# Kernel tuning notes

Measured on AMD Instinct MI355X. Metric: run time of the kernel, lower is better.

Reference implementation:

```python
import jax, jax.numpy as jnp
import numpy as np

B, N, H, W = 128, 8192, 7, 7


def setup_inputs() -> dict:
    key = jax.random.key(0)
    ks = jax.random.split(key, 10)
    inp = {
        'x': jax.random.normal(ks[0], (B, N, H, W), dtype=jnp.float32),
        'y': jax.random.normal(ks[1], (B, N), dtype=jnp.float32),
        # nn.MultiheadAttention(embed_dim=1, num_heads=1) params (all scalar)
        'wq': jax.random.normal(ks[2], (), dtype=jnp.float32),
        'wk': jax.random.normal(ks[3], (), dtype=jnp.float32),
        'wv': jax.random.normal(ks[4], (), dtype=jnp.float32),
        'bq': jax.random.normal(ks[5], (), dtype=jnp.float32) * 0.1,
        'bk': jax.random.normal(ks[6], (), dtype=jnp.float32) * 0.1,
        'bv': jax.random.normal(ks[7], (), dtype=jnp.float32) * 0.1,
        'wo': jax.random.normal(ks[8], (), dtype=jnp.float32),
        'bo': jax.random.normal(ks[9], (), dtype=jnp.float32) * 0.1,
    }
    return inp


def _mha1(q_src, kv_src, wq, bq, wk, bk, wv, bv, wo, bo):
    # embed_dim=1, num_heads=1, scale = 1/sqrt(1) = 1.
    # torch sees (seq=B, batch=N, embed=1): attention mixes the B axis per n.
    q = q_src * wq + bq            # [B, N]
    k = kv_src * wk + bk           # [B, N]
    v = kv_src * wv + bv           # [B, N]
    scores = jnp.einsum('in,jn->ijn', q, k)      # [B, B, N]
    a = jax.nn.softmax(scores, axis=1)           # softmax over keys j
    out = jnp.einsum('ijn,jn->in', a, v)         # [B, N]
    return out * wo + bo


def reference(x, y, wq, bq, wk, bk, wv, bv, wo, bo):
    xp = jnp.mean(x, axis=(2, 3))                # AdaptiveAvgPool2d((1,1)) -> [B, N]
    self_x = _mha1(xp, xp, wq, bq, wk, bk, wv, bv, wo, bo)
    self_y = _mha1(y, y, wq, bq, wk, bk, wv, bv, wo, bo)
    cross_x = _mha1(xp, y, wq, bq, wk, bk, wv, bv, wo, bo)
    cross_y = _mha1(y, xp, wq, bq, wk, bk, wv, bv, wo, bo)
    f_x = xp + self_x
    f_y = y + self_y
    c_f_x = cross_x + f_x
    c_f_y = cross_y + f_y
    return jnp.concatenate((c_f_x, c_f_y), axis=1)   # [B, 2N]
```

## Files before the change

kernel.cpp:

```cpp
#include <hip/hip_runtime.h>


constexpr int B_SEQ = 128;
constexpr int N_COL = 8192;
constexpr int HWP   = 49;
constexpr int NT    = 256;
constexpr int TC    = 4;
constexpr int PC    = 128;

__global__ __launch_bounds__(NT) void rsca_pool(
    const float* __restrict__ x, float* __restrict__ xp)
{
    __shared__ float st[PC * HWP];
    const int t = threadIdx.x;
    const int ntiles = (B_SEQ * N_COL) / PC;
    for (int tile = blockIdx.x; tile < ntiles; tile += gridDim.x) {
        const size_t cell0 = (size_t)tile * PC;
        const float4* src = (const float4*)(x + cell0 * HWP);
        __syncthreads();
        for (int k = t; k < PC * HWP / 4; k += NT)
            ((float4*)st)[k] = src[k];
        __syncthreads();
        const int cell = t >> 1, half = t & 1;
        const float* p = st + cell * HWP + half * 25;
        float s = 0.0f;
        #pragma unroll
        for (int k = 0; k < 24; ++k) s += p[k];
        if (half == 0) s += p[24];
        s += __shfl_xor(s, 1);
        if (half == 0) xp[cell0 + cell] = s * (1.0f / HWP);
    }
}

__global__ __launch_bounds__(NT, 6) void rsca_attn(
    const float* __restrict__ xp, const float* __restrict__ y,
    const float* __restrict__ pwq, const float* __restrict__ pwk,
    const float* __restrict__ pwv, const float* __restrict__ pbq,
    const float* __restrict__ pbk, const float* __restrict__ pbv,
    const float* __restrict__ pwo, const float* __restrict__ pbo,
    float* __restrict__ out)
{
    __shared__ float2 kvxT[TC][B_SEQ];
    __shared__ float2 kvyT[TC][B_SEQ];
    __shared__ float  pmn[2][TC][8], pmx[2][TC][8];
    __shared__ float  klmn[2][TC], klmx[2][TC];

    const int t  = threadIdx.x;
    const int n0 = blockIdx.x * TC;

    const float wq = pwq[0], wk = pwk[0], wv = pwv[0];
    const float bq = pbq[0], bk = pbk[0], bv = pbv[0];
    const float wo = pwo[0], bo = pbo[0];
    const float L2E = 1.4426950408889634f;
    const float wkL = wk * L2E, bkL = bk * L2E;
    const float alpha = wo * wv;
    const float beta2 = 2.0f * (wo * bv + bo);

    for (int cell = t; cell < B_SEQ * TC; cell += NT) {
        const int j = cell >> 2, c = cell & 3;
        const float fx = xp[(size_t)j * N_COL + n0 + c];
        const float fy = y [(size_t)j * N_COL + n0 + c];
        kvxT[c][j] = make_float2(fmaf(fx, wkL, bkL), fx);
        kvyT[c][j] = make_float2(fmaf(fy, wkL, bkL), fy);
    }
    __syncthreads();

    if (t < 64) {
        const int set = t >> 5, c = (t >> 3) & 3, part = t & 7;
        float mn = 3.4e38f, mx = -3.4e38f;
        #pragma unroll
        for (int k = 0; k < 16; ++k) {
            const int j = part * 16 + k;
            const float v = set ? kvyT[c][j].x : kvxT[c][j].x;
            mn = fminf(mn, v);
            mx = fmaxf(mx, v);
        }
        pmn[set][c][part] = mn;
        pmx[set][c][part] = mx;
    }
    __syncthreads();
    if (t < 8) {
        const int set = t >> 2, c = t & 3;
        float mn = 3.4e38f, mx = -3.4e38f;
        #pragma unroll
        for (int k = 0; k < 8; ++k) {
            mn = fminf(mn, pmn[set][c][k]);
            mx = fmaxf(mx, pmx[set][c][k]);
        }
        klmn[set][c] = mn;
        klmx[set][c] = mx;
    }
    __syncthreads();

    const int i  = t & (B_SEQ - 1);
    const int ch = t >> 7;
    #pragma unroll
    for (int cc = 0; cc < 2; ++cc) {
        const int c = ch * 2 + cc;
        const float2* __restrict__ px = kvxT[c];
        const float2* __restrict__ py = kvyT[c];
        const float xi = px[i].y;
        const float yi = py[i].y;
        const float qx = fmaf(xi, wq, bq);
        const float qy = fmaf(yi, wq, bq);
        const float nmsx = -(qx >= 0.0f ? qx * klmx[0][c] : qx * klmn[0][c]);
        const float nmcy = -(qy >= 0.0f ? qy * klmx[0][c] : qy * klmn[0][c]);
        const float nmsy = -(qy >= 0.0f ? qy * klmx[1][c] : qy * klmn[1][c]);
        const float nmcx = -(qx >= 0.0f ? qx * klmx[1][c] : qx * klmn[1][c]);

        float s0sx = 0.f, s1sx = 0.f, s0cy = 0.f, s1cy = 0.f;
        float s0sy = 0.f, s1sy = 0.f, s0cx = 0.f, s1cx = 0.f;
        for (int j0 = 0; j0 < B_SEQ; j0 += 8) {
            float2 kx[8], ky[8];
            #pragma unroll
            for (int jj = 0; jj < 8; ++jj) kx[jj] = px[j0 + jj];
            #pragma unroll
            for (int jj = 0; jj < 8; ++jj) ky[jj] = py[j0 + jj];
            #pragma unroll
            for (int jj = 0; jj < 8; ++jj) {
                const float e1 = __builtin_amdgcn_exp2f(fmaf(qx, kx[jj].x, nmsx));
                const float e2 = __builtin_amdgcn_exp2f(fmaf(qy, kx[jj].x, nmcy));
                const float e3 = __builtin_amdgcn_exp2f(fmaf(qy, ky[jj].x, nmsy));
                const float e4 = __builtin_amdgcn_exp2f(fmaf(qx, ky[jj].x, nmcx));
                s1sx = fmaf(e1, kx[jj].y, s1sx); s0sx += e1;
                s1cy = fmaf(e2, kx[jj].y, s1cy); s0cy += e2;
                s1sy = fmaf(e3, ky[jj].y, s1sy); s0sy += e3;
                s1cx = fmaf(e4, ky[jj].y, s1cx); s0cx += e4;
            }
        }
        const float mx_attn = s1sx * __builtin_amdgcn_rcpf(s0sx)
                            + s1cx * __builtin_amdgcn_rcpf(s0cx);
        const float my_attn = s1sy * __builtin_amdgcn_rcpf(s0sy)
                            + s1cy * __builtin_amdgcn_rcpf(s0cy);
        out[(size_t)i * (2 * N_COL) + n0 + c]         = fmaf(alpha, mx_attn, beta2 + xi);
        out[(size_t)i * (2 * N_COL) + N_COL + n0 + c] = fmaf(alpha, my_attn, beta2 + yi);
    }
}

extern "C" void kernel_launch(void* const* d_in, const int* in_sizes, int n_in,
                              void* d_out, int out_size, void* d_ws, size_t ws_size,
                              hipStream_t stream) {
    const float* x   = (const float*)d_in[0];
    const float* y   = (const float*)d_in[1];
    const float* pwq = (const float*)d_in[2];
    const float* pwk = (const float*)d_in[3];
    const float* pwv = (const float*)d_in[4];
    const float* pbq = (const float*)d_in[5];
    const float* pbk = (const float*)d_in[6];
    const float* pbv = (const float*)d_in[7];
    const float* pwo = (const float*)d_in[8];
    const float* pbo = (const float*)d_in[9];
    float* xp  = (float*)d_ws;
    float* out = (float*)d_out;

    rsca_pool<<<dim3(2048), dim3(NT), 0, stream>>>(x, xp);
    rsca_attn<<<dim3(N_COL / TC), dim3(NT), 0, stream>>>(
        xp, y, pwq, pwk, pwv, pbq, pbk, pbv, pwo, pbo, out);
}
```

Before: 377.5 us.

## Fuse spatial average pooling into attention kernel, dropping xp workspace

Measured after the change: 333.1 us. 1.13x faster.

```diff
diff --git a/kernel.cpp b/kernel.cpp
--- a/kernel.cpp
+++ b/kernel.cpp
@@ -6,34 +6,9 @@
 constexpr int HWP   = 49;
 constexpr int NT    = 256;
 constexpr int TC    = 4;
-constexpr int PC    = 128;
 
-__global__ __launch_bounds__(NT) void rsca_pool(
-    const float* __restrict__ x, float* __restrict__ xp)
-{
-    __shared__ float st[PC * HWP];
-    const int t = threadIdx.x;
-    const int ntiles = (B_SEQ * N_COL) / PC;
-    for (int tile = blockIdx.x; tile < ntiles; tile += gridDim.x) {
-        const size_t cell0 = (size_t)tile * PC;
-        const float4* src = (const float4*)(x + cell0 * HWP);
-        __syncthreads();
-        for (int k = t; k < PC * HWP / 4; k += NT)
-            ((float4*)st)[k] = src[k];
-        __syncthreads();
-        const int cell = t >> 1, half = t & 1;
-        const float* p = st + cell * HWP + half * 25;
-        float s = 0.0f;
-        #pragma unroll
-        for (int k = 0; k < 24; ++k) s += p[k];
-        if (half == 0) s += p[24];
-        s += __shfl_xor(s, 1);
-        if (half == 0) xp[cell0 + cell] = s * (1.0f / HWP);
-    }
-}
-
-__global__ __launch_bounds__(NT, 6) void rsca_attn(
-    const float* __restrict__ xp, const float* __restrict__ y,
+__global__ __launch_bounds__(NT, 4) void rsca_fused(
+    const float* __restrict__ x, const float* __restrict__ y,
     const float* __restrict__ pwq, const float* __restrict__ pwk,
     const float* __restrict__ pwv, const float* __restrict__ pbq,
     const float* __restrict__ pbk, const float* __restrict__ pbv,
@@ -58,10 +33,51 @@
 
     for (int cell = t; cell < B_SEQ * TC; cell += NT) {
         const int j = cell >> 2, c = cell & 3;
-        const float fx = xp[(size_t)j * N_COL + n0 + c];
-        const float fy = y [(size_t)j * N_COL + n0 + c];
-        kvxT[c][j] = make_float2(fmaf(fx, wkL, bkL), fx);
+        const float fy = y[(size_t)j * N_COL + n0 + c];
         kvyT[c][j] = make_float2(fmaf(fy, wkL, bkL), fy);
+    }
+
+    const int ql  = t & 3;
+    const int seg = t >> 2;
+    for (int pass = 0; pass < 2; ++pass) {
+        const int j = pass * 64 + seg;
+        const float4* __restrict__ base =
+            (const float4*)(x + ((size_t)j * N_COL + n0) * (size_t)HWP);
+        float s0 = 0.f, s1 = 0.f, s2 = 0.f, s3 = 0.f;
+        float4 v;
+        v = base[ql +  0]; s0 += v.x + v.y + v.z + v.w;
+        v = base[ql +  4]; s0 += v.x + v.y + v.z + v.w;
+        v = base[ql +  8]; s0 += v.x + v.y + v.z + v.w;
+        v = base[ql + 16]; s1 += v.x + v.y + v.z + v.w;
+        v = base[ql + 20]; s1 += v.x + v.y + v.z + v.w;
+        v = base[ql + 28]; s2 += v.x + v.y + v.z + v.w;
+        v = base[ql + 32]; s2 += v.x + v.y + v.z + v.w;
+        v = base[ql + 40]; s3 += v.x + v.y + v.z + v.w;
+        v = base[ql + 44]; s3 += v.x + v.y + v.z + v.w;
+        v = base[ql + 12];
+        { const float sm = v.x + v.y + v.z + v.w;
+          const float cr = (ql == 0) ? v.x : 0.0f;
+          s0 += cr; s1 += sm - cr; }
+        v = base[ql + 24];
+        { const float sm = v.x + v.y + v.z + v.w;
+          const float cr = (ql == 0) ? (v.x + v.y) : 0.0f;
+          s1 += cr; s2 += sm - cr; }
+        v = base[ql + 36];
+        { const float sm = v.x + v.y + v.z + v.w;
+          const float cr = (ql == 0) ? (v.x + v.y + v.z) : 0.0f;
+          s2 += cr; s3 += sm - cr; }
+        v = base[48];
+        const float tail = v.x + v.y + v.z + v.w;
+        s0 += __shfl_xor(s0, 1); s1 += __shfl_xor(s1, 1);
+        s2 += __shfl_xor(s2, 1); s3 += __shfl_xor(s3, 1);
+        s0 += __shfl_xor(s0, 2); s1 += __shfl_xor(s1, 2);
+        s2 += __shfl_xor(s2, 2); s3 += __shfl_xor(s3, 2);
+        float r = s0;
+        r = (ql == 1) ? s1 : r;
+        r = (ql == 2) ? s2 : r;
+        r = (ql == 3) ? (s3 + tail) : r;
+        const float mean = r * (1.0f / HWP);
+        kvxT[ql][j] = make_float2(fmaf(mean, wkL, bkL), mean);
     }
     __syncthreads();
 
@@ -71,9 +87,9 @@
         #pragma unroll
         for (int k = 0; k < 16; ++k) {
             const int j = part * 16 + k;
-            const float v = set ? kvyT[c][j].x : kvxT[c][j].x;
-            mn = fminf(mn, v);
-            mx = fmaxf(mx, v);
+            const float vv = set ? kvyT[c][j].x : kvxT[c][j].x;
+            mn = fminf(mn, vv);
+            mx = fmaxf(mx, vv);
         }
         pmn[set][c][part] = mn;
         pmx[set][c][part] = mx;
@@ -150,10 +166,8 @@
     const float* pbv = (const float*)d_in[7];
     const float* pwo = (const float*)d_in[8];
     const float* pbo = (const float*)d_in[9];
-    float* xp  = (float*)d_ws;
     float* out = (float*)d_out;
 
-    rsca_pool<<<dim3(2048), dim3(NT), 0, stream>>>(x, xp);
-    rsca_attn<<<dim3(N_COL / TC), dim3(NT), 0, stream>>>(
-        xp, y, pwq, pwk, pwv, pbq, pbk, pbv, pwo, pbo, out);
+    rsca_fused<<<dim3(N_COL / TC), dim3(NT), 0, stream>>>(
+        x, y, pwq, pwk, pwv, pbq, pbk, pbv, pwo, pbo, out);
 }
```
